# Performance work log

Hardware: AMD Instinct MI355X
Metric: run time of the kernel (lower is better)

The kernel has to match this reference:

```python
import jax, jax.numpy as jnp
import numpy as np

IN_FEATURES = 4096
OUT_FEATURES = 11008
TOKENS = 2048  # batch*seq flattened


def setup_inputs() -> dict:
    key = jax.random.key(0)
    k_x, k_w, k_s, k_z, k_b = jax.random.split(key, 5)
    x = jax.random.normal(k_x, (TOKENS, IN_FEATURES), dtype=jnp.float32)
    qweight = jax.random.randint(k_w, (OUT_FEATURES, IN_FEATURES), 0, 256, dtype=jnp.int32).astype(jnp.uint8)
    # realistic small positive scales, zero points in mid-range
    scale = jax.random.uniform(k_s, (OUT_FEATURES, 1), dtype=jnp.float32, minval=0.001, maxval=0.02)
    zero_point = jax.random.uniform(k_z, (OUT_FEATURES, 1), dtype=jnp.float32, minval=0.0, maxval=255.0)
    bias = jax.random.normal(k_b, (OUT_FEATURES,), dtype=jnp.float32)
    return {"x": x, "qweight": qweight, "scale": scale, "zero_point": zero_point, "bias": bias}


def reference(x, qweight, scale, zero_point, bias) -> jnp.ndarray:
    # dequantize: (q - zp) * s, per output channel  -> [out, in]
    w = (qweight.astype(scale.dtype) - zero_point) * scale
    # F.linear: x @ w.T + bias -> [tokens, out]
    return jnp.einsum("ti,oi->to", x, w) + bias
```

## Files before the change

kernel.cpp:

```cpp
#include <hip/hip_runtime.h>
#include <hip/hip_bf16.h>
#include <stdint.h>

typedef __bf16 bf16_t;
typedef bf16_t bf16x8 __attribute__((ext_vector_type(8)));
typedef float  f32x4  __attribute__((ext_vector_type(4)));
typedef int    i32x4  __attribute__((ext_vector_type(4)));

#define M_TOK 2048
#define N_OUT 11008
#define K_IN  4096
#define N16   (N_OUT / 16)
#define NTILE 1376

__global__ __launch_bounds__(256)
void prep(const int* __restrict__ Q, const float* __restrict__ X,
          signed char* __restrict__ W8t, signed char* __restrict__ X8t,
          float* __restrict__ dxv, float* __restrict__ sxv)
{
    __shared__ float wmax[4];
    __shared__ int   wsum[4];
    const int tid = threadIdx.x;

    if (blockIdx.x < N16) {
        const int n16 = blockIdx.x;
        const int fr  = tid & 15;
        const int fg  = (tid >> 4) & 3;
        const int w   = tid >> 6;
        const int* qrow = Q + (size_t)(n16 * 16 + fr) * K_IN + fg * 16;
        signed char* wout = W8t + ((size_t)n16 * 64 + (tid & 63)) * 16;
        #pragma unroll 4
        for (int kt2 = 0; kt2 < 16; ++kt2) {
            const int kt = kt2 * 4 + w;
            const int4* q4 = (const int4*)(qrow + kt * 64);
            unsigned int pk[4];
            #pragma unroll
            for (int j = 0; j < 4; ++j) {
                const int4 q = q4[j];
                pk[j] =  (unsigned int)((q.x - 128) & 255)
                      | ((unsigned int)((q.y - 128) & 255) << 8)
                      | ((unsigned int)((q.z - 128) & 255) << 16)
                      | ((unsigned int)((q.w - 128) & 255) << 24);
            }
            *(int4*)(wout + (size_t)kt * (N16 * 1024)) = *(const int4*)pk;
        }
        return;
    }

    const int row = blockIdx.x - N16;
    const float* xr = X + (size_t)row * K_IN + tid * 16;
    float v[16];
    #pragma unroll
    for (int j = 0; j < 4; ++j)
        *(float4*)(v + j * 4) = ((const float4*)xr)[j];

    float amax = 0.f;
    #pragma unroll
    for (int j = 0; j < 16; ++j) amax = fmaxf(amax, fabsf(v[j]));
    #pragma unroll
    for (int m = 1; m < 64; m <<= 1)
        amax = fmaxf(amax, __shfl_xor(amax, m));
    const int wv = tid >> 6;
    if ((tid & 63) == 0) wmax[wv] = amax;
    __syncthreads();
    amax = fmaxf(fmaxf(wmax[0], wmax[1]), fmaxf(wmax[2], wmax[3]));
    amax = fmaxf(amax, 1e-20f);
    const float inv = 127.f / amax;

    int sum = 0;
    unsigned int pk[4];
    #pragma unroll
    for (int j = 0; j < 4; ++j) {
        unsigned int p = 0;
        #pragma unroll
        for (int i = 0; i < 4; ++i) {
            int xi = (int)__builtin_rintf(v[j * 4 + i] * inv);
            xi = max(-127, min(127, xi));
            sum += xi;
            p |= ((unsigned int)(xi & 255)) << (8 * i);
        }
        pk[j] = p;
    }
    const size_t toff = (((size_t)(tid >> 2) * 128 + (row >> 4)) * 64
                         + (size_t)((tid & 3) * 16 + (row & 15))) * 16;
    *(int4*)(X8t + toff) = *(const int4*)pk;

    #pragma unroll
    for (int m = 1; m < 64; m <<= 1) sum += __shfl_xor(sum, m);
    if ((tid & 63) == 0) wsum[wv] = sum;
    __syncthreads();
    if (tid == 0) {
        dxv[row] = amax * (1.f / 127.f);
        sxv[row] = (float)(wsum[0] + wsum[1] + wsum[2] + wsum[3]);
    }
}


#define LOAD_A4(DA, KT) do {                                                   \
    const char* ap_ = gAt + (size_t)(KT) * (128 * 1024);                       \
    DA##0 = *(const i32x4*)(ap_ + 0 * 1024);                                   \
    DA##1 = *(const i32x4*)(ap_ + 1 * 1024);                                   \
    DA##2 = *(const i32x4*)(ap_ + 2 * 1024);                                   \
    DA##3 = *(const i32x4*)(ap_ + 3 * 1024);                                   \
} while (0)

#define LOAD_B4(DB, KT) do {                                                   \
    const char* bp_ = gBt + (size_t)(KT) * (N16 * 1024);                       \
    DB##0 = *(const i32x4*)(bp_ + 0 * 1024);                                   \
    DB##1 = *(const i32x4*)(bp_ + 1 * 1024);                                   \
    DB##2 = *(const i32x4*)(bp_ + 2 * 1024);                                   \
    DB##3 = *(const i32x4*)(bp_ + 3 * 1024);                                   \
} while (0)

#define MMQ(FA, FB, MQ, NQ)                                                    \
    acc[MQ][NQ] = __builtin_amdgcn_mfma_i32_16x16x64_i8(FA##MQ, FB##NQ, acc[MQ][NQ], 0, 0, 0)

#define MFMA16(FA, FB) do {                                                    \
    __builtin_amdgcn_s_setprio(1);                                             \
    MMQ(FA, FB, 0, 0); MMQ(FA, FB, 0, 1); MMQ(FA, FB, 0, 2); MMQ(FA, FB, 0, 3);\
    MMQ(FA, FB, 1, 0); MMQ(FA, FB, 1, 1); MMQ(FA, FB, 1, 2); MMQ(FA, FB, 1, 3);\
    MMQ(FA, FB, 2, 0); MMQ(FA, FB, 2, 1); MMQ(FA, FB, 2, 2); MMQ(FA, FB, 2, 3);\
    MMQ(FA, FB, 3, 0); MMQ(FA, FB, 3, 1); MMQ(FA, FB, 3, 2); MMQ(FA, FB, 3, 3);\
    __builtin_amdgcn_s_setprio(0);                                             \
} while (0)

#define REGION17(CA, CB, NA, NB, KTN) do {                                     \
    LOAD_A4(NA, KTN);                                                          \
    LOAD_B4(NB, KTN);                                                          \
    MFMA16(CA, CB);                                                            \
} while (0)

__global__ __launch_bounds__(256)
void gemm_i8(const signed char* __restrict__ A8t,
             const signed char* __restrict__ B8t,
             const float* __restrict__ dxv,
             const float* __restrict__ sxv,
             const float* __restrict__ S,
             const float* __restrict__ Z,
             const float* __restrict__ Bias,
             float* __restrict__ O)
{
    const int tid  = threadIdx.x;
    const int lane = tid & 63;
    const int wid  = tid >> 6;
    const int wr   = wid >> 1;
    const int wc   = wid & 1;
    const int fr   = lane & 15;
    const int fg   = lane >> 4;

    const int bid = blockIdx.x;
    const int xcd = bid & 7;
    const int k   = bid >> 3;
    int col, by;
    if (k < 160) { col = 10 * xcd + (k >> 4); by = k & 15; }
    else         { const int g = xcd * 12 + (k - 160); col = 80 + (g >> 4); by = g & 15; }
    const long bm = (long)by * 128;
    const long bn = (long)col * 128;

    const char* gAt = (const char*)A8t
                    + (((size_t)(by * 8 + wr * 4)) * 64 + lane) * 16;
    const char* gBt = (const char*)B8t
                    + (((size_t)(col * 8 + wc * 4)) * 64 + lane) * 16;

    i32x4 acc[4][4] = {};
    i32x4 pa0, pa1, pa2, pa3, pb0, pb1, pb2, pb3;
    i32x4 qa0, qa1, qa2, qa3, qb0, qb1, qb2, qb3;

    LOAD_A4(pa, 0);
    LOAD_B4(pb, 0);

    #pragma unroll 1
    for (int i = 0; i < 31; ++i) {
        REGION17(pa, pb, qa, qb, 2 * i + 1);
        REGION17(qa, qb, pa, pb, 2 * i + 2);
    }
    REGION17(pa, pb, qa, qb, 63);
    MFMA16(qa, qb);

    float dxa[16], sxa[16];
    #pragma unroll
    for (int m = 0; m < 4; ++m)
        #pragma unroll
        for (int r = 0; r < 4; ++r) {
            const int row = (int)bm + wr * 64 + m * 16 + (fg << 2) + r;
            dxa[m * 4 + r] = dxv[row];
            sxa[m * 4 + r] = sxv[row];
        }
    #pragma unroll
    for (int n = 0; n < 4; ++n) {
        const long ocol = bn + wc * 64 + n * 16 + fr;
        const float s  = S[ocol];
        const float f  = 128.f - Z[ocol];
        const float bi = Bias[ocol];
        #pragma unroll
        for (int m = 0; m < 4; ++m) {
            const long row0 = bm + wr * 64 + m * 16 + (fg << 2);
            #pragma unroll
            for (int r = 0; r < 4; ++r) {
                const float g = (float)acc[m][n][r] + f * sxa[m * 4 + r];
                O[(size_t)(row0 + r) * N_OUT + ocol] = s * dxa[m * 4 + r] * g + bi;
            }
        }
    }
}

__global__ __launch_bounds__(256)
void qlinear_fused(const float* __restrict__ X,
                   const int*   __restrict__ Q,
                   const float* __restrict__ S,
                   const float* __restrict__ Z,
                   const float* __restrict__ Bias,
                   float* __restrict__ O)
{
    __shared__ bf16_t As[128][32];
    __shared__ bf16_t Bs[128][32];
    const int tid = threadIdx.x, lane = tid & 63, wid = tid >> 6;
    const int wr = wid >> 1, wc = wid & 1, fr = lane & 15, fg = lane >> 4;
    const int bm = blockIdx.y * 128, bn = blockIdx.x * 128;
    const int srow = tid >> 1, scol = (tid & 1) << 4;
    const float s_n = S[bn + srow];
    const float zs_n = Z[bn + srow] * s_n;
    const float* xptr = X + (size_t)(bm + srow) * K_IN + scol;
    const int*   qptr = Q + (size_t)(bn + srow) * K_IN + scol;
    f32x4 acc[4][4] = {};
    for (int k0 = 0; k0 < K_IN; k0 += 32) {
        float a[16]; int qi[16];
        { const float4* s4 = (const float4*)(xptr + k0);
          *(float4*)(a+0)=s4[0]; *(float4*)(a+4)=s4[1]; *(float4*)(a+8)=s4[2]; *(float4*)(a+12)=s4[3]; }
        { const int4* s4 = (const int4*)(qptr + k0);
          *(int4*)(qi+0)=s4[0]; *(int4*)(qi+4)=s4[1]; *(int4*)(qi+8)=s4[2]; *(int4*)(qi+12)=s4[3]; }
        float b[16];
        #pragma unroll
        for (int j = 0; j < 16; ++j) b[j] = (float)qi[j] * s_n - zs_n;
        bf16x8 pa0, pa1, pb0, pb1;
        #pragma unroll
        for (int j = 0; j < 8; ++j) {
            pa0[j]=(bf16_t)a[j]; pa1[j]=(bf16_t)a[j+8];
            pb0[j]=(bf16_t)b[j]; pb1[j]=(bf16_t)b[j+8];
        }
        *(bf16x8*)&As[srow][scol]   = pa0; *(bf16x8*)&As[srow][scol+8] = pa1;
        *(bf16x8*)&Bs[srow][scol]   = pb0; *(bf16x8*)&Bs[srow][scol+8] = pb1;
        __syncthreads();
        bf16x8 af[4], bfv[4];
        #pragma unroll
        for (int m = 0; m < 4; ++m) af[m] = *(const bf16x8*)&As[wr*64+m*16+fr][fg*8];
        #pragma unroll
        for (int n = 0; n < 4; ++n) bfv[n] = *(const bf16x8*)&Bs[wc*64+n*16+fr][fg*8];
        #pragma unroll
        for (int m = 0; m < 4; ++m)
            #pragma unroll
            for (int n = 0; n < 4; ++n)
                acc[m][n] = __builtin_amdgcn_mfma_f32_16x16x32_bf16(af[m], bfv[n], acc[m][n], 0,0,0);
        __syncthreads();
    }
    #pragma unroll
    for (int n = 0; n < 4; ++n) {
        const int col = bn + wc*64 + n*16 + fr;
        const float bv = Bias[col];
        #pragma unroll
        for (int m = 0; m < 4; ++m) {
            const int row0 = bm + wr*64 + m*16 + fg*4;
            #pragma unroll
            for (int r = 0; r < 4; ++r)
                O[(size_t)(row0 + r) * N_OUT + col] = acc[m][n][r] + bv;
        }
    }
}

extern "C" void kernel_launch(void* const* d_in, const int* in_sizes, int n_in,
                              void* d_out, int out_size, void* d_ws, size_t ws_size,
                              hipStream_t stream) {
    const float* X    = (const float*)d_in[0];
    const int*   Q    = (const int*)d_in[1];
    const float* S    = (const float*)d_in[2];
    const float* Z    = (const float*)d_in[3];
    const float* Bias = (const float*)d_in[4];
    float* O = (float*)d_out;

    const size_t wbytes = (size_t)N_OUT * K_IN;
    const size_t xbytes = (size_t)M_TOK * K_IN;
    const size_t need   = wbytes + xbytes + 2 * M_TOK * sizeof(float) + 256;

    if (ws_size >= need) {
        signed char* W8t = (signed char*)d_ws;
        signed char* X8t = (signed char*)d_ws + wbytes;
        float* dxv = (float*)((char*)d_ws + wbytes + xbytes);
        float* sxv = dxv + M_TOK;
        prep<<<dim3(N16 + M_TOK), 256, 0, stream>>>(Q, X, W8t, X8t, dxv, sxv);
        gemm_i8<<<dim3(NTILE), 256, 0, stream>>>(X8t, W8t, dxv, sxv, S, Z, Bias, O);
    } else {
        dim3 grid(N_OUT / 128, M_TOK / 128);
        qlinear_fused<<<grid, 256, 0, stream>>>(X, Q, S, Z, Bias, O);
    }
}
```

Measured before the change: 193.1 us.

## Widen int8 GEMM tile to 128x256 with half-step B register pipeline

Doubles the per-block N tile from 128 to 256 columns, so each wave computes a 64x128 output with 4x8 accumulators. A fragments are reused across two B halves, and B is streamed in half-K-step chunks through a four-deep register rotation. The XCD-aware block mapping is redone for half as many tiles, and launch bounds now request two blocks per CU. This cuts A reloads and global traffic per MFMA, at the cost of much higher register pressure and fewer blocks to balance across CUs.

```diff
diff --git a/kernel.cpp b/kernel.cpp
--- a/kernel.cpp
+++ b/kernel.cpp
@@ -11,7 +11,7 @@
 #define N_OUT 11008
 #define K_IN  4096
 #define N16   (N_OUT / 16)
-#define NTILE 1376
+#define NTILE 688
 
 __global__ __launch_bounds__(256)
 void prep(const int* __restrict__ Q, const float* __restrict__ X,
@@ -104,33 +104,33 @@
     DA##3 = *(const i32x4*)(ap_ + 3 * 1024);                                   \
 } while (0)
 
-#define LOAD_B4(DB, KT) do {                                                   \
-    const char* bp_ = gBt + (size_t)(KT) * (N16 * 1024);                       \
-    DB##0 = *(const i32x4*)(bp_ + 0 * 1024);                                   \
-    DB##1 = *(const i32x4*)(bp_ + 1 * 1024);                                   \
-    DB##2 = *(const i32x4*)(bp_ + 2 * 1024);                                   \
-    DB##3 = *(const i32x4*)(bp_ + 3 * 1024);                                   \
+#define LOAD_BH(BS, H) do {                                                    \
+    const char* bp_ = gBt + (size_t)((H) >> 1) * (N16 * 1024)                  \
+                          + (size_t)((H) & 1) * 4096;                          \
+    BS##0 = *(const i32x4*)(bp_ + 0 * 1024);                                   \
+    BS##1 = *(const i32x4*)(bp_ + 1 * 1024);                                   \
+    BS##2 = *(const i32x4*)(bp_ + 2 * 1024);                                   \
+    BS##3 = *(const i32x4*)(bp_ + 3 * 1024);                                   \
 } while (0)
 
-#define MMQ(FA, FB, MQ, NQ)                                                    \
-    acc[MQ][NQ] = __builtin_amdgcn_mfma_i32_16x16x64_i8(FA##MQ, FB##NQ, acc[MQ][NQ], 0, 0, 0)
-
-#define MFMA16(FA, FB) do {                                                    \
+#define MMH(FA, BS, MQ, NH, NQ)                                                \
+    acc[MQ][(NH) * 4 + (NQ)] = __builtin_amdgcn_mfma_i32_16x16x64_i8(          \
+        FA##MQ, BS##NQ, acc[MQ][(NH) * 4 + (NQ)], 0, 0, 0)
+
+#define MFMA16H(FA, BS, NH) do {                                               \
     __builtin_amdgcn_s_setprio(1);                                             \
-    MMQ(FA, FB, 0, 0); MMQ(FA, FB, 0, 1); MMQ(FA, FB, 0, 2); MMQ(FA, FB, 0, 3);\
-    MMQ(FA, FB, 1, 0); MMQ(FA, FB, 1, 1); MMQ(FA, FB, 1, 2); MMQ(FA, FB, 1, 3);\
-    MMQ(FA, FB, 2, 0); MMQ(FA, FB, 2, 1); MMQ(FA, FB, 2, 2); MMQ(FA, FB, 2, 3);\
-    MMQ(FA, FB, 3, 0); MMQ(FA, FB, 3, 1); MMQ(FA, FB, 3, 2); MMQ(FA, FB, 3, 3);\
+    MMH(FA, BS, 0, NH, 0); MMH(FA, BS, 0, NH, 1);                              \
+    MMH(FA, BS, 0, NH, 2); MMH(FA, BS, 0, NH, 3);                              \
+    MMH(FA, BS, 1, NH, 0); MMH(FA, BS, 1, NH, 1);                              \
+    MMH(FA, BS, 1, NH, 2); MMH(FA, BS, 1, NH, 3);                              \
+    MMH(FA, BS, 2, NH, 0); MMH(FA, BS, 2, NH, 1);                              \
+    MMH(FA, BS, 2, NH, 2); MMH(FA, BS, 2, NH, 3);                              \
+    MMH(FA, BS, 3, NH, 0); MMH(FA, BS, 3, NH, 1);                              \
+    MMH(FA, BS, 3, NH, 2); MMH(FA, BS, 3, NH, 3);                              \
     __builtin_amdgcn_s_setprio(0);                                             \
 } while (0)
 
-#define REGION17(CA, CB, NA, NB, KTN) do {                                     \
-    LOAD_A4(NA, KTN);                                                          \
-    LOAD_B4(NB, KTN);                                                          \
-    MFMA16(CA, CB);                                                            \
-} while (0)
-
-__global__ __launch_bounds__(256)
+__global__ __launch_bounds__(256, 2)
 void gemm_i8(const signed char* __restrict__ A8t,
              const signed char* __restrict__ B8t,
              const float* __restrict__ dxv,
@@ -152,30 +152,41 @@
     const int xcd = bid & 7;
     const int k   = bid >> 3;
     int col, by;
-    if (k < 160) { col = 10 * xcd + (k >> 4); by = k & 15; }
-    else         { const int g = xcd * 12 + (k - 160); col = 80 + (g >> 4); by = g & 15; }
+    if (k < 80) { col = 5 * xcd + (k >> 4); by = k & 15; }
+    else        { const int e = k - 80; col = 40 + (e >> 1); by = 2 * xcd + (e & 1); }
     const long bm = (long)by * 128;
-    const long bn = (long)col * 128;
+    const long bn = (long)col * 256;
 
     const char* gAt = (const char*)A8t
                     + (((size_t)(by * 8 + wr * 4)) * 64 + lane) * 16;
     const char* gBt = (const char*)B8t
-                    + (((size_t)(col * 8 + wc * 4)) * 64 + lane) * 16;
-
-    i32x4 acc[4][4] = {};
-    i32x4 pa0, pa1, pa2, pa3, pb0, pb1, pb2, pb3;
-    i32x4 qa0, qa1, qa2, qa3, qb0, qb1, qb2, qb3;
-
+                    + (((size_t)(col * 16 + wc * 8)) * 64 + lane) * 16;
+
+    i32x4 acc[4][8] = {};
+    i32x4 pa0, pa1, pa2, pa3, qa0, qa1, qa2, qa3;
+    i32x4 b00, b01, b02, b03;
+    i32x4 b10, b11, b12, b13;
+    i32x4 b20, b21, b22, b23;
+    i32x4 b30, b31, b32, b33;
+
+    LOAD_BH(b0, 0);
+    LOAD_BH(b1, 1);
+    LOAD_BH(b2, 2);
     LOAD_A4(pa, 0);
-    LOAD_B4(pb, 0);
+    LOAD_A4(qa, 1);
 
     #pragma unroll 1
     for (int i = 0; i < 31; ++i) {
-        REGION17(pa, pb, qa, qb, 2 * i + 1);
-        REGION17(qa, qb, pa, pb, 2 * i + 2);
-    }
-    REGION17(pa, pb, qa, qb, 63);
-    MFMA16(qa, qb);
+        const int h = 4 * i;
+        LOAD_BH(b3, h + 3); MFMA16H(pa, b0, 0);
+        LOAD_BH(b0, h + 4); MFMA16H(pa, b1, 1); LOAD_A4(pa, 2 * i + 2);
+        LOAD_BH(b1, h + 5); MFMA16H(qa, b2, 0);
+        LOAD_BH(b2, h + 6); MFMA16H(qa, b3, 1); LOAD_A4(qa, 2 * i + 3);
+    }
+    LOAD_BH(b3, 127); MFMA16H(pa, b0, 0);
+    MFMA16H(pa, b1, 1);
+    MFMA16H(qa, b2, 0);
+    MFMA16H(qa, b3, 1);
 
     float dxa[16], sxa[16];
     #pragma unroll
@@ -187,8 +198,8 @@
             sxa[m * 4 + r] = sxv[row];
         }
     #pragma unroll
-    for (int n = 0; n < 4; ++n) {
-        const long ocol = bn + wc * 64 + n * 16 + fr;
+    for (int n = 0; n < 8; ++n) {
+        const long ocol = bn + wc * 128 + n * 16 + fr;
         const float s  = S[ocol];
         const float f  = 128.f - Z[ocol];
         const float bi = Bias[ocol];
```

After: 172.3 us. 10.8% less time.
